# Performance work log

Hardware: AMD Instinct MI355X
Metric: run time of the kernel (lower is better)

Reference implementation:

```python
import jax, jax.numpy as jnp
import numpy as np

B, S, H = 1024, 16, 1024
N = 16384          # retrieved neighbors per user
L = 128            # num_labels


def setup_inputs() -> dict:
    key = jax.random.key(0)
    ks = jax.random.split(key, 6)
    features = jax.random.normal(ks[0], (B, S, H), dtype=jnp.float32)
    sims = jax.random.uniform(ks[1], (B, N), dtype=jnp.float32)
    labels = jax.random.randint(ks[2], (B, N), 0, L, dtype=jnp.int32)
    dense_w = jax.random.normal(ks[3], (H, H + L), dtype=jnp.float32) * 0.02
    dense_b = jnp.zeros((H,), dtype=jnp.float32)
    out_w = jax.random.normal(ks[4], (L, H), dtype=jnp.float32) * 0.02
    out_b = jnp.zeros((L,), dtype=jnp.float32)
    return {
        "features": features,
        "user_texts_similarities": sims,
        "user_texts_labels": labels,
        "dense_w": dense_w,
        "dense_b": dense_b,
        "out_w": out_w,
        "out_b": out_b,
    }


def _aggregate_labels(sims, labels):
    # mean over N of one_hot(labels) * sims  ->  scatter-add then divide.
    b, n = sims.shape
    agg = jnp.zeros((b, L), dtype=sims.dtype)
    rows = jnp.arange(b, dtype=jnp.int32)[:, None]  # [B,1] broadcast against [B,N]
    agg = agg.at[rows, labels].add(sims)
    return agg / n  # [B, L]


def reference(features, user_texts_similarities, user_texts_labels,
              dense_w, dense_b, out_w, out_b):
    # top_k=None, normalize_weights=False, feature_normalization='none', eval (dropout=id)
    agg = _aggregate_labels(user_texts_similarities, user_texts_labels)  # [B, L]
    cls = features[:, 0, :]                                              # [B, H]
    x = jnp.concatenate((cls, agg), axis=1)                              # [B, H+L]
    x = jnp.tanh(x @ dense_w.T + dense_b)                                # [B, H]
    return x @ out_w.T + out_b                                           # [B, L]
```

## Files before the change

kernel.cpp:

```cpp
#include <hip/hip_runtime.h>

#define B_DIM 1024
#define S_DIM 16
#define H_DIM 1024
#define N_DIM 16384
#define L_DIM 128
#define KX    (H_DIM + L_DIM)

typedef __bf16 bf16_8 __attribute__((ext_vector_type(8)));
typedef float  f32x4  __attribute__((ext_vector_type(4)));

__device__ __forceinline__ unsigned short f2bf(float f) {
    unsigned int u = __float_as_uint(f);
    u += 0x7fffu + ((u >> 16) & 1u);
    return (unsigned short)(u >> 16);
}

#define GLD16(gp, lp)                                                          \
    __builtin_amdgcn_global_load_lds(                                          \
        (const __attribute__((address_space(1))) void*)(gp),                   \
        (__attribute__((address_space(3))) void*)(lp), 16, 0, 0)

__global__ __launch_bounds__(256) void k_agg(
    const float* __restrict__ feats,
    const float* __restrict__ sims,
    const int*   __restrict__ labels,
    unsigned short* __restrict__ xin)
{
    __shared__ float bins[64][L_DIM + 1];
    const int b = blockIdx.x;
    const int t = threadIdx.x;
    const int c = t >> 2;

    float* flat = (float*)bins;
    for (int i = t; i < 64 * (L_DIM + 1); i += 256) flat[i] = 0.f;
    __syncthreads();

    const float4* s4 = (const float4*)(sims   + (size_t)b * N_DIM);
    const int4*   l4 = (const int4*)  (labels + (size_t)b * N_DIM);
    #pragma unroll 4
    for (int v = t; v < N_DIM / 4; v += 256) {
        float4 s  = s4[v];
        int4   li = l4[v];
        atomicAdd(&bins[c][li.x], s.x);
        atomicAdd(&bins[c][li.y], s.y);
        atomicAdd(&bins[c][li.z], s.z);
        atomicAdd(&bins[c][li.w], s.w);
    }
    __syncthreads();

    unsigned short* xrow = xin + (size_t)b * KX;
    const float4* c4 = (const float4*)(feats + (size_t)b * (S_DIM * H_DIM));
    float4 cv = c4[t];
    ushort4 p;
    p.x = f2bf(cv.x); p.y = f2bf(cv.y); p.z = f2bf(cv.z); p.w = f2bf(cv.w);
    *(ushort4*)(xrow + t * 4) = p;

    if (t < L_DIM) {
        float s = 0.f;
        #pragma unroll
        for (int cc = 0; cc < 64; ++cc) s += bins[cc][t];
        xrow[H_DIM + t] = f2bf(s * (1.0f / N_DIM));
    }
}

__global__ __launch_bounds__(256) void k_cvt(
    const float* __restrict__ w1, const float* __restrict__ w2,
    unsigned short* __restrict__ o1, unsigned short* __restrict__ o2,
    int n1v, int n2v)
{
    int idx = blockIdx.x * 256 + threadIdx.x;
    int stride = gridDim.x * 256;
    for (int i = idx; i < n1v + n2v; i += stride) {
        const float4* src; unsigned short* dst; int j;
        if (i < n1v) { src = (const float4*)w1; dst = o1; j = i; }
        else         { src = (const float4*)w2; dst = o2; j = i - n1v; }
        float4 v = src[j];
        ushort4 p;
        p.x = f2bf(v.x); p.y = f2bf(v.y); p.z = f2bf(v.z); p.w = f2bf(v.w);
        *(ushort4*)(dst + j * 4) = p;
    }
}

template <int EPI>
__global__ __launch_bounds__(256) void k_gemm_bt(
    const unsigned short* __restrict__ A,
    const unsigned short* __restrict__ Bm,
    const float* __restrict__ bias,
    void* __restrict__ Cout,
    int M, int N, int K, int ldc)
{
    __shared__ __align__(16) unsigned short sm[3][2][64 * 64];

    const int t    = threadIdx.x;
    const int lane = t & 63;
    const int w    = t >> 6;
    const int wm   = w >> 1, wn = w & 1;
    const int m0   = blockIdx.y * 64;
    const int n0   = blockIdx.x * 64;
    const int lr   = lane & 15;
    const int hi   = lane >> 4;

    int srcj[2];
    #pragma unroll
    for (int j = 0; j < 2; ++j) {
        int li  = t + j * 256;
        int row = li >> 3;
        int g   = li & 7;
        int gs  = g ^ (row & 7);
        srcj[j] = row * K + gs * 8;
    }
    const size_t aBase = (size_t)m0 * K;
    const size_t bBase = (size_t)n0 * K;

    const int nt = K >> 6;
    f32x4 acc[2][2] = {};

#define STAGE(buf, k0_)                                                        \
    do {                                                                       \
        _Pragma("unroll")                                                      \
        for (int j = 0; j < 2; ++j) {                                          \
            int li = t + j * 256;                                              \
            GLD16(A  + aBase + (size_t)(srcj[j] + (k0_)), &sm[buf][0][li * 8]);\
            GLD16(Bm + bBase + (size_t)(srcj[j] + (k0_)), &sm[buf][1][li * 8]);\
        }                                                                      \
    } while (0)

    STAGE(0, 0);
    if (nt > 1) STAGE(1, 64);

    int cur = 0;
    for (int ti = 0; ti < nt; ++ti) {
        int b2 = cur + 2; if (b2 >= 3) b2 -= 3;
        if (ti + 2 < nt) {
            STAGE(b2, (ti + 2) << 6);
            asm volatile("s_waitcnt vmcnt(8)" ::: "memory");
        } else if (ti + 1 < nt) {
            asm volatile("s_waitcnt vmcnt(4)" ::: "memory");
        } else {
            asm volatile("s_waitcnt vmcnt(0)" ::: "memory");
        }
        __builtin_amdgcn_s_barrier();
        asm volatile("" ::: "memory");

        const unsigned short* As = sm[cur][0];
        const unsigned short* Bs = sm[cur][1];
        #pragma unroll
        for (int ks = 0; ks < 2; ++ks) {
            const int gl = ks * 4 + hi;
            const int ga = (gl ^ (lr & 7)) * 8;
            bf16_8 a0 = *(const bf16_8*)(As + (wm * 32 +      lr) * 64 + ga);
            bf16_8 a1 = *(const bf16_8*)(As + (wm * 32 + 16 + lr) * 64 + ga);
            bf16_8 b0 = *(const bf16_8*)(Bs + (wn * 32 +      lr) * 64 + ga);
            bf16_8 b1 = *(const bf16_8*)(Bs + (wn * 32 + 16 + lr) * 64 + ga);
            acc[0][0] = __builtin_amdgcn_mfma_f32_16x16x32_bf16(a0, b0, acc[0][0], 0, 0, 0);
            acc[0][1] = __builtin_amdgcn_mfma_f32_16x16x32_bf16(a0, b1, acc[0][1], 0, 0, 0);
            acc[1][0] = __builtin_amdgcn_mfma_f32_16x16x32_bf16(a1, b0, acc[1][0], 0, 0, 0);
            acc[1][1] = __builtin_amdgcn_mfma_f32_16x16x32_bf16(a1, b1, acc[1][1], 0, 0, 0);
        }

        asm volatile("" ::: "memory");
        __builtin_amdgcn_s_barrier();
        cur = cur + 1; if (cur >= 3) cur = 0;
    }

    const int rbase = m0 + wm * 32 + hi * 4;
    const int cbase = n0 + wn * 32 + lr;
    #pragma unroll
    for (int i = 0; i < 2; ++i) {
        #pragma unroll
        for (int j = 0; j < 2; ++j) {
            int col = cbase + j * 16;
            float bv = bias[col];
            #pragma unroll
            for (int r = 0; r < 4; ++r) {
                int row = rbase + i * 16 + r;
                float v = acc[i][j][r] + bv;
                if (EPI == 0) {
                    v = tanhf(v);
                    ((unsigned short*)Cout)[(size_t)row * ldc + col] = f2bf(v);
                } else {
                    ((float*)Cout)[(size_t)row * ldc + col] = v;
                }
            }
        }
    }
#undef STAGE
}

extern "C" void kernel_launch(void* const* d_in, const int* in_sizes, int n_in,
                              void* d_out, int out_size, void* d_ws, size_t ws_size,
                              hipStream_t stream) {
    const float* feats   = (const float*)d_in[0];
    const float* sims    = (const float*)d_in[1];
    const int*   labels  = (const int*)  d_in[2];
    const float* dense_w = (const float*)d_in[3];
    const float* dense_b = (const float*)d_in[4];
    const float* out_w   = (const float*)d_in[5];
    const float* out_b   = (const float*)d_in[6];
    float* out = (float*)d_out;

    unsigned short* xin  = (unsigned short*)d_ws;
    unsigned short* wd   = xin  + (size_t)B_DIM * KX;
    unsigned short* wo   = wd   + (size_t)H_DIM * KX;
    unsigned short* xmid = wo   + (size_t)L_DIM * H_DIM;

    k_agg<<<B_DIM, 256, 0, stream>>>(feats, sims, labels, xin);

    int n1v = (H_DIM * KX) / 4;
    int n2v = (L_DIM * H_DIM) / 4;
    k_cvt<<<512, 256, 0, stream>>>(dense_w, out_w, wd, wo, n1v, n2v);

    dim3 g1(H_DIM / 64, B_DIM / 64);
    k_gemm_bt<0><<<g1, 256, 0, stream>>>(xin, wd, dense_b, (void*)xmid,
                                         B_DIM, H_DIM, KX, H_DIM);

    dim3 g2(L_DIM / 64, B_DIM / 64);
    k_gemm_bt<1><<<g2, 256, 0, stream>>>(xmid, wo, out_b, (void*)out,
                                         B_DIM, L_DIM, H_DIM, L_DIM);
}
```

Measured before the change: 247.7 us.

## Shrink GEMM N-tile to 32 and transpose aggregation bins for conflict-free atomics

```diff
diff --git a/kernel.cpp b/kernel.cpp
--- a/kernel.cpp
+++ b/kernel.cpp
@@ -27,13 +27,14 @@
     const int*   __restrict__ labels,
     unsigned short* __restrict__ xin)
 {
-    __shared__ float bins[64][L_DIM + 1];
+    __shared__ float binsT[L_DIM][64];
     const int b = blockIdx.x;
     const int t = threadIdx.x;
-    const int c = t >> 2;
-
-    float* flat = (float*)bins;
-    for (int i = t; i < 64 * (L_DIM + 1); i += 256) flat[i] = 0.f;
+    const int c = t & 63;
+
+    float* flat = (float*)binsT;
+    #pragma unroll
+    for (int i = 0; i < L_DIM * 64 / 256; ++i) flat[t + i * 256] = 0.f;
     __syncthreads();
 
     const float4* s4 = (const float4*)(sims   + (size_t)b * N_DIM);
@@ -42,10 +43,10 @@
     for (int v = t; v < N_DIM / 4; v += 256) {
         float4 s  = s4[v];
         int4   li = l4[v];
-        atomicAdd(&bins[c][li.x], s.x);
-        atomicAdd(&bins[c][li.y], s.y);
-        atomicAdd(&bins[c][li.z], s.z);
-        atomicAdd(&bins[c][li.w], s.w);
+        atomicAdd(&binsT[li.x][c], s.x);
+        atomicAdd(&binsT[li.y][c], s.y);
+        atomicAdd(&binsT[li.z][c], s.z);
+        atomicAdd(&binsT[li.w][c], s.w);
     }
     __syncthreads();
 
@@ -59,7 +60,7 @@
     if (t < L_DIM) {
         float s = 0.f;
         #pragma unroll
-        for (int cc = 0; cc < 64; ++cc) s += bins[cc][t];
+        for (int i = 0; i < 64; ++i) s += binsT[t][(i + t) & 63];
         xrow[H_DIM + t] = f2bf(s * (1.0f / N_DIM));
     }
 }
@@ -90,39 +91,43 @@
     void* __restrict__ Cout,
     int M, int N, int K, int ldc)
 {
-    __shared__ __align__(16) unsigned short sm[3][2][64 * 64];
+    __shared__ __align__(16) unsigned short smA[3][64 * 64];
+    __shared__ __align__(16) unsigned short smB[3][32 * 64];
 
     const int t    = threadIdx.x;
     const int lane = t & 63;
     const int w    = t >> 6;
     const int wm   = w >> 1, wn = w & 1;
     const int m0   = blockIdx.y * 64;
-    const int n0   = blockIdx.x * 64;
+    const int n0   = blockIdx.x * 32;
     const int lr   = lane & 15;
     const int hi   = lane >> 4;
 
-    int srcj[2];
+    int srcA[2];
     #pragma unroll
     for (int j = 0; j < 2; ++j) {
         int li  = t + j * 256;
         int row = li >> 3;
-        int g   = li & 7;
-        int gs  = g ^ (row & 7);
-        srcj[j] = row * K + gs * 8;
-    }
+        int g   = (li & 7) ^ (row & 7);
+        srcA[j] = row * K + g * 8;
+    }
+    const int rowB = t >> 3;
+    const int gB   = (t & 7) ^ (rowB & 7);
+    const int srcB = rowB * K + gB * 8;
+
     const size_t aBase = (size_t)m0 * K;
     const size_t bBase = (size_t)n0 * K;
 
     const int nt = K >> 6;
-    f32x4 acc[2][2] = {};
+    f32x4 acc[2] = {};
 
 #define STAGE(buf, k0_)                                                        \
     do {                                                                       \
+        GLD16(Bm + bBase + (size_t)(srcB + (k0_)), &smB[buf][t * 8]);          \
         _Pragma("unroll")                                                      \
         for (int j = 0; j < 2; ++j) {                                          \
             int li = t + j * 256;                                              \
-            GLD16(A  + aBase + (size_t)(srcj[j] + (k0_)), &sm[buf][0][li * 8]);\
-            GLD16(Bm + bBase + (size_t)(srcj[j] + (k0_)), &sm[buf][1][li * 8]);\
+            GLD16(A + aBase + (size_t)(srcA[j] + (k0_)), &smA[buf][li * 8]);   \
         }                                                                      \
     } while (0)
 
@@ -134,29 +139,26 @@
         int b2 = cur + 2; if (b2 >= 3) b2 -= 3;
         if (ti + 2 < nt) {
             STAGE(b2, (ti + 2) << 6);
-            asm volatile("s_waitcnt vmcnt(8)" ::: "memory");
+            asm volatile("s_waitcnt vmcnt(6)" ::: "memory");
         } else if (ti + 1 < nt) {
-            asm volatile("s_waitcnt vmcnt(4)" ::: "memory");
+            asm volatile("s_waitcnt vmcnt(3)" ::: "memory");
         } else {
             asm volatile("s_waitcnt vmcnt(0)" ::: "memory");
         }
         __builtin_amdgcn_s_barrier();
         asm volatile("" ::: "memory");
 
-        const unsigned short* As = sm[cur][0];
-        const unsigned short* Bs = sm[cur][1];
+        const unsigned short* As = smA[cur];
+        const unsigned short* Bs = smB[cur];
         #pragma unroll
         for (int ks = 0; ks < 2; ++ks) {
             const int gl = ks * 4 + hi;
             const int ga = (gl ^ (lr & 7)) * 8;
             bf16_8 a0 = *(const bf16_8*)(As + (wm * 32 +      lr) * 64 + ga);
             bf16_8 a1 = *(const bf16_8*)(As + (wm * 32 + 16 + lr) * 64 + ga);
-            bf16_8 b0 = *(const bf16_8*)(Bs + (wn * 32 +      lr) * 64 + ga);
-            bf16_8 b1 = *(const bf16_8*)(Bs + (wn * 32 + 16 + lr) * 64 + ga);
-            acc[0][0] = __builtin_amdgcn_mfma_f32_16x16x32_bf16(a0, b0, acc[0][0], 0, 0, 0);
-            acc[0][1] = __builtin_amdgcn_mfma_f32_16x16x32_bf16(a0, b1, acc[0][1], 0, 0, 0);
-            acc[1][0] = __builtin_amdgcn_mfma_f32_16x16x32_bf16(a1, b0, acc[1][0], 0, 0, 0);
-            acc[1][1] = __builtin_amdgcn_mfma_f32_16x16x32_bf16(a1, b1, acc[1][1], 0, 0, 0);
+            bf16_8 b0 = *(const bf16_8*)(Bs + (wn * 16 +      lr) * 64 + ga);
+            acc[0] = __builtin_amdgcn_mfma_f32_16x16x32_bf16(a0, b0, acc[0], 0, 0, 0);
+            acc[1] = __builtin_amdgcn_mfma_f32_16x16x32_bf16(a1, b0, acc[1], 0, 0, 0);
         }
 
         asm volatile("" ::: "memory");
@@ -165,23 +167,19 @@
     }
 
     const int rbase = m0 + wm * 32 + hi * 4;
-    const int cbase = n0 + wn * 32 + lr;
+    const int col   = n0 + wn * 16 + lr;
+    const float bv  = bias[col];
     #pragma unroll
     for (int i = 0; i < 2; ++i) {
         #pragma unroll
-        for (int j = 0; j < 2; ++j) {
-            int col = cbase + j * 16;
-            float bv = bias[col];
-            #pragma unroll
-            for (int r = 0; r < 4; ++r) {
-                int row = rbase + i * 16 + r;
-                float v = acc[i][j][r] + bv;
-                if (EPI == 0) {
-                    v = tanhf(v);
-                    ((unsigned short*)Cout)[(size_t)row * ldc + col] = f2bf(v);
-                } else {
-                    ((float*)Cout)[(size_t)row * ldc + col] = v;
-                }
+        for (int r = 0; r < 4; ++r) {
+            int row = rbase + i * 16 + r;
+            float v = acc[i][r] + bv;
+            if (EPI == 0) {
+                v = tanhf(v);
+                ((unsigned short*)Cout)[(size_t)row * ldc + col] = f2bf(v);
+            } else {
+                ((float*)Cout)[(size_t)row * ldc + col] = v;
             }
         }
     }
@@ -211,11 +209,11 @@
     int n2v = (L_DIM * H_DIM) / 4;
     k_cvt<<<512, 256, 0, stream>>>(dense_w, out_w, wd, wo, n1v, n2v);
 
-    dim3 g1(H_DIM / 64, B_DIM / 64);
+    dim3 g1(H_DIM / 32, B_DIM / 64);
     k_gemm_bt<0><<<g1, 256, 0, stream>>>(xin, wd, dense_b, (void*)xmid,
                                          B_DIM, H_DIM, KX, H_DIM);
 
-    dim3 g2(L_DIM / 64, B_DIM / 64);
+    dim3 g2(L_DIM / 32, B_DIM / 64);
     k_gemm_bt<1><<<g2, 256, 0, stream>>>(xmid, wo, out_b, (void*)out,
                                          B_DIM, L_DIM, H_DIM, L_DIM);
 }
```

Result: slower. 254.8 us (+2.9%).
